# Optimization experiments

Hardware: AMD Instinct MI355X
Metric: run time of the kernel (lower is better)

The kernel has to match this reference:

```python
import jax, jax.numpy as jnp
import numpy as np

DIM = 768
NUM_HEADS = 12
HEAD_DIM = DIM // NUM_HEADS
SCALE = HEAD_DIM ** -0.5


def setup_inputs() -> dict:
    key = jax.random.key(0)
    k1, k2, k3, k4, k5 = jax.random.split(key, 5)
    B, N = 8, 2048
    x = jax.random.normal(k1, (B, N, DIM), dtype=jnp.float32)
    mask = jax.random.randint(k2, (B, N), 0, 2, dtype=jnp.int32)
    # ensure at least one valid key per batch row to avoid all -inf softmax rows
    mask = mask.at[:, 0].set(1)
    w_qkv = jax.random.normal(k3, (DIM, 3 * DIM), dtype=jnp.float32) * (DIM ** -0.5)
    w_proj = jax.random.normal(k4, (DIM, DIM), dtype=jnp.float32) * (DIM ** -0.5)
    b_proj = jax.random.normal(k5, (DIM,), dtype=jnp.float32) * 0.02
    return {"x": x, "mask": mask, "w_qkv": w_qkv, "w_proj": w_proj, "b_proj": b_proj}


def reference(x, mask, w_qkv, w_proj, b_proj):
    B, N, C = x.shape
    qkv = (x @ w_qkv).reshape(B, N, 3, NUM_HEADS, HEAD_DIM)
    qkv = jnp.transpose(qkv, (2, 0, 3, 1, 4))  # [3, B, H, N, D]
    q, k, v = qkv[0], qkv[1], qkv[2]
    q = q * SCALE
    # fp32 upcast for scores (inputs already fp32; explicit for fidelity)
    attn = jnp.einsum('bhqd,bhkd->bhqk', q.astype(jnp.float32), k.astype(jnp.float32))
    key_mask = mask.astype(bool)[:, None, None, :]  # [B,1,1,N]
    attn = jnp.where(key_mask, attn, -jnp.inf)
    attn = jax.nn.softmax(attn, axis=-1).astype(x.dtype)
    out = jnp.einsum('bhqk,bhkd->bhqd', attn, v)  # [B,H,N,D]
    out = jnp.transpose(out, (0, 2, 1, 3)).reshape(B, N, C)
    return out @ w_proj + b_proj
```

## Files before the change

### kernel.cpp

```cpp
#include <hip/hip_runtime.h>
#include <hip/hip_bf16.h>
#include <stdint.h>

#define NHEAD 12
#define SEQ   2048
#define NB    8
#define MTOK  (NB*SEQ)
#define DIMC  768
#define QKVN  (3*DIMC)

typedef __attribute__((ext_vector_type(8))) short bf16x8;
typedef __attribute__((ext_vector_type(4))) float f32x4;
typedef __attribute__((ext_vector_type(16))) float f32x16;
typedef __attribute__((ext_vector_type(4))) unsigned short u16x4;
typedef __attribute__((ext_vector_type(4))) unsigned int u32x4;

typedef const __attribute__((address_space(1))) char glb_char;
typedef __attribute__((address_space(3))) char lds_char;

__device__ __forceinline__ unsigned short f2bf(float f) {
  union { float f; unsigned u; } v; v.f = f;
  return (unsigned short)((v.u + 0x7FFFu + ((v.u >> 16) & 1u)) >> 16);
}

__device__ __forceinline__ void gload_lds16(const void* g, void* l) {
  __builtin_amdgcn_global_load_lds((glb_char*)g, (lds_char*)l, 16, 0, 0);
}

__device__ __forceinline__ unsigned cvtpk_bf16(float lo, float hi) {
  unsigned d;
  asm("v_cvt_pk_bf16_f32 %0, %1, %2" : "=v"(d) : "v"(lo), "v"(hi));
  return d;
}

#define QSCALE 0.18033688011112042f
#define MASKBIAS -30000.0f

__global__ void __launch_bounds__(256, 8)
cvt_bf16_kernel(const float* __restrict__ in,
                unsigned short* __restrict__ out, int n4) {
  int idx = blockIdx.x * blockDim.x + threadIdx.x;
  int stride = gridDim.x * blockDim.x;
  for (int i = idx; i < n4; i += stride) {
    float4 v = ((const float4*)in)[i];
    u16x4 o;
    o.x = f2bf(v.x); o.y = f2bf(v.y); o.z = f2bf(v.z); o.w = f2bf(v.w);
    ((u16x4*)out)[i] = o;
  }
}

__global__ void __launch_bounds__(256, 4)
maskscan_kernel(const int* __restrict__ mask, int* __restrict__ posmap,
                int* __restrict__ srcidx, float* __restrict__ mbias_c,
                int* __restrict__ nvalid) {
  __shared__ int sums[256];
  __shared__ int btot;
  const int b = blockIdx.x, t = threadIdx.x;
  const int* m = mask + b * SEQ;
  int loc[8];
  int s = 0;
  #pragma unroll
  for (int i = 0; i < 8; i++) { loc[i] = (m[t * 8 + i] != 0) ? 1 : 0; s += loc[i]; }
  sums[t] = s;
  __syncthreads();
  for (int off = 1; off < 256; off <<= 1) {
    int v = (t >= off) ? sums[t - off] : 0;
    __syncthreads();
    sums[t] += v;
    __syncthreads();
  }
  int excl = sums[t] - s;
  if (t == 255) btot = sums[255];
  __syncthreads();
  const int nv = btot;
  #pragma unroll
  for (int i = 0; i < 8; i++) {
    posmap[b * SEQ + t * 8 + i] = loc[i] ? excl : -1;
    if (loc[i]) srcidx[b * SEQ + excl] = t * 8 + i;
    excl += loc[i];
  }
  for (int j = t; j < SEQ; j += 256) {
    mbias_c[b * SEQ + j] = (j < nv) ? 0.0f : MASKBIAS;
    if (j >= nv) srcidx[b * SEQ + j] = 0;
  }
  if (t == 0) nvalid[b] = nv;
}

__global__ void __launch_bounds__(256, 8)
transpose_cvt2_kernel(const float* __restrict__ in0, unsigned short* __restrict__ out0,
                      const float* __restrict__ in1, unsigned short* __restrict__ out1) {
  __shared__ float tile[32][33];
  const int z = blockIdx.z;
  const float* in = z ? in1 : in0;
  unsigned short* out = z ? out1 : out0;
  const int C = z ? DIMC : QKVN;
  const int R = DIMC;
  int c0 = blockIdx.x * 32, r0 = blockIdx.y * 32;
  if (c0 >= C) return;
  int tx = threadIdx.x & 31, ty = threadIdx.x >> 5;
  #pragma unroll
  for (int i = 0; i < 32; i += 8)
    tile[ty + i][tx] = in[(size_t)(r0 + ty + i) * C + c0 + tx];
  __syncthreads();
  #pragma unroll
  for (int i = 0; i < 32; i += 8)
    out[(size_t)(c0 + ty + i) * R + r0 + tx] = f2bf(tile[tx][ty + i]);
}

__global__ void __launch_bounds__(256, 3)
qkv_gemm_kernel(const unsigned short* __restrict__ xb,
                const unsigned short* __restrict__ wT,
                unsigned short* __restrict__ qo,
                unsigned short* __restrict__ ko,
                unsigned short* __restrict__ vto,
                const int* __restrict__ srcidx,
                const int* __restrict__ nvalid) {
  __shared__ short lA[3][128 * 32];
  __shared__ short lB[3][128 * 32];
  const int t = threadIdx.x;
  const int lane = t & 63, w = t >> 6;
  const int wr = (w >> 1) * 64, wc = (w & 1) * 64;
  const int l15 = lane & 15, lg = lane >> 4;
  const int sr = t >> 2;
  const int sc = t & 3;
  const int z = blockIdx.z;
  const int NT = DIMC / 32;

  if (z < NB) {
    const int b = z;
    const int m0 = blockIdx.x * 128;
    if (m0 >= ((nvalid[b] + 127) & ~127)) return;
    const int n0 = blockIdx.y * 128;

    const int srow0 = srcidx[b * SEQ + m0 + sr];
    const int srow1 = srcidx[b * SEQ + m0 + 64 + sr];
    const unsigned short* xbb = xb + (size_t)b * SEQ * DIMC;
    const unsigned short* wTkv = wT + (size_t)DIMC * DIMC;

    auto STAGE = [&](int k0, int bsel) {
      int cb = (sc ^ ((sr >> 1) & 3)) * 8;
      gload_lds16(xbb + (size_t)srow0 * DIMC + k0 + cb,
                  (char*)lA + bsel * 8192 + w * 1024);
      gload_lds16(xbb + (size_t)srow1 * DIMC + k0 + cb,
                  (char*)lA + bsel * 8192 + 4096 + w * 1024);
      #pragma unroll
      for (int i = 0; i < 2; i++) {
        int row = i * 64 + sr;
        int cb2 = (sc ^ ((row >> 1) & 3)) * 8;
        gload_lds16(wTkv + (size_t)(n0 + row) * DIMC + k0 + cb2,
                    (char*)lB + bsel * 8192 + i * 4096 + w * 1024);
      }
    };

    f32x4 acc[4][4] = {};
    STAGE(0, 0);
    STAGE(32, 1);
    int cur = 0;
    for (int kt = 0; kt < NT; ++kt) {
      if (kt < NT - 1) asm volatile("s_waitcnt vmcnt(4)" ::: "memory");
      else             asm volatile("s_waitcnt vmcnt(0)" ::: "memory");
      __builtin_amdgcn_s_barrier();
      if (kt + 2 < NT) {
        int nb = cur + 2; if (nb >= 3) nb -= 3;
        STAGE((kt + 2) * 32, nb);
      }
      const short* A = &lA[cur][0];
      const short* B = &lB[cur][0];

      bf16x8 af[4], bfr[4];
      #pragma unroll
      for (int mi = 0; mi < 4; mi++) {
        int m = wr + mi * 16 + l15;
        af[mi] = *(const bf16x8*)&A[m * 32 + ((lg ^ ((m >> 1) & 3)) << 3)];
      }
      #pragma unroll
      for (int nj = 0; nj < 4; nj++) {
        int n = wc + nj * 16 + l15;
        bfr[nj] = *(const bf16x8*)&B[n * 32 + ((lg ^ ((n >> 1) & 3)) << 3)];
      }
      __builtin_amdgcn_s_setprio(1);
      #pragma unroll
      for (int mi = 0; mi < 4; mi++)
        #pragma unroll
        for (int nj = 0; nj < 4; nj++)
          acc[mi][nj] = __builtin_amdgcn_mfma_f32_16x16x32_bf16(af[mi], bfr[nj], acc[mi][nj], 0, 0, 0);
      __builtin_amdgcn_s_setprio(0);

      cur = (cur == 2) ? 0 : cur + 1;
    }

    #pragma unroll
    for (int mi = 0; mi < 4; mi++) {
      int pos0 = m0 + wr + mi * 16 + 4 * lg;
      #pragma unroll
      for (int nj = 0; nj < 4; nj++) {
        int col = n0 + wc + nj * 16 + l15;
        int ch = (col >= DIMC) ? col - DIMC : col;
        int hh = ch >> 6, dd = ch & 63;
        size_t hb = (size_t)(b * NHEAD + hh);
        if (col < DIMC) {
          size_t base = (hb * SEQ + pos0) * 64 + dd;
          #pragma unroll
          for (int r = 0; r < 4; r++)
            ko[base + (size_t)r * 64] = f2bf(acc[mi][nj][r]);
        } else {
          size_t base = (hb * 64 + dd) * SEQ + pos0;
          u16x4 pk;
          pk.x = f2bf(acc[mi][nj][0]); pk.y = f2bf(acc[mi][nj][1]);
          pk.z = f2bf(acc[mi][nj][2]); pk.w = f2bf(acc[mi][nj][3]);
          *(u16x4*)(vto + base) = pk;
        }
      }
    }
  } else {
    const int id = (z - NB) * 192 + blockIdx.y * 16 + blockIdx.x;
    const int m0 = (id / 6) * 128;
    const int n0 = (id % 6) * 128;

    auto STAGE = [&](int k0, int bsel) {
      #pragma unroll
      for (int i = 0; i < 2; i++) {
        int row = i * 64 + sr;
        int cb = (sc ^ ((row >> 1) & 3)) * 8;
        gload_lds16(xb + (size_t)(m0 + row) * DIMC + k0 + cb,
                    (char*)lA + bsel * 8192 + i * 4096 + w * 1024);
        gload_lds16(wT + (size_t)(n0 + row) * DIMC + k0 + cb,
                    (char*)lB + bsel * 8192 + i * 4096 + w * 1024);
      }
    };

    f32x4 acc[4][4] = {};
    STAGE(0, 0);
    STAGE(32, 1);
    int cur = 0;
    for (int kt = 0; kt < NT; ++kt) {
      if (kt < NT - 1) asm volatile("s_waitcnt vmcnt(4)" ::: "memory");
      else             asm volatile("s_waitcnt vmcnt(0)" ::: "memory");
      __builtin_amdgcn_s_barrier();
      if (kt + 2 < NT) {
        int nb = cur + 2; if (nb >= 3) nb -= 3;
        STAGE((kt + 2) * 32, nb);
      }
      const short* A = &lA[cur][0];
      const short* B = &lB[cur][0];

      bf16x8 af[4], bfr[4];
      #pragma unroll
      for (int mi = 0; mi < 4; mi++) {
        int m = wr + mi * 16 + l15;
        af[mi] = *(const bf16x8*)&A[m * 32 + ((lg ^ ((m >> 1) & 3)) << 3)];
      }
      #pragma unroll
      for (int nj = 0; nj < 4; nj++) {
        int n = wc + nj * 16 + l15;
        bfr[nj] = *(const bf16x8*)&B[n * 32 + ((lg ^ ((n >> 1) & 3)) << 3)];
      }
      __builtin_amdgcn_s_setprio(1);
      #pragma unroll
      for (int mi = 0; mi < 4; mi++)
        #pragma unroll
        for (int nj = 0; nj < 4; nj++)
          acc[mi][nj] = __builtin_amdgcn_mfma_f32_16x16x32_bf16(af[mi], bfr[nj], acc[mi][nj], 0, 0, 0);
      __builtin_amdgcn_s_setprio(0);

      cur = (cur == 2) ? 0 : cur + 1;
    }

    #pragma unroll
    for (int mi = 0; mi < 4; mi++) {
      int tok0 = m0 + wr + mi * 16 + 4 * lg;
      int bb = tok0 >> 11;
      int nn0 = tok0 & 2047;
      #pragma unroll
      for (int nj = 0; nj < 4; nj++) {
        int col = n0 + wc + nj * 16 + l15;
        int hh = col >> 6, dd = col & 63;
        size_t base = (((size_t)(bb * NHEAD + hh)) * SEQ + nn0) * 64 + dd;
        #pragma unroll
        for (int r = 0; r < 4; r++)
          qo[base + (size_t)r * 64] = f2bf(acc[mi][nj][r] * QSCALE);
      }
    }
  }
}

__global__ void __launch_bounds__(256, 4)
attn_kernel(const unsigned short* __restrict__ qbuf,
            const unsigned short* __restrict__ kbuf,
            const unsigned short* __restrict__ vtbuf,
            const float* __restrict__ mbias_c,
            const int* __restrict__ nvalid,
            unsigned short* __restrict__ ao) {
  __shared__ short lKV[2][8192];
  __shared__ float lmask[2][64];
  const int t = threadIdx.x, lane = t & 63, w = t >> 6;
  const int l31 = lane & 31, hi = lane >> 5;
  const int bid = blockIdx.x;
  const int qt = bid / 96;
  const int bh = bid - qt * 96;
  const int b = bh / NHEAD, h = bh - b * NHEAD;
  const int q0 = qt * 128 + w * 32;
  const unsigned short* qb = qbuf + (size_t)bh * SEQ * 64;
  const unsigned short* kb = kbuf + (size_t)bh * SEQ * 64;
  const unsigned short* vb = vtbuf + (size_t)bh * 64 * SEQ;
  const float* mb = mbias_c + b * SEQ;
  const int ntiles = (nvalid[b] + 63) >> 6;

  auto STAGE = [&](int tile, int bsel) {
    int kv0 = tile * 64;
    #pragma unroll
    for (int i = 0; i < 2; i++) {
      int c = i * 4 + w;
      gload_lds16(kb + (size_t)(kv0 + lane) * 64 + c * 8,
                  (char*)lKV + bsel * 16384 + c * 1024);
      gload_lds16(vb + (size_t)lane * SEQ + kv0 + c * 8,
                  (char*)lKV + bsel * 16384 + 8192 + c * 1024);
    }
    if (w == 0)
      __builtin_amdgcn_global_load_lds((glb_char*)(mb + tile * 64 + lane),
                                       (lds_char*)&lmask[bsel][0], 4, 0, 0);
  };

  bf16x8 qf[4];
  #pragma unroll
  for (int dblk = 0; dblk < 4; dblk++)
    qf[dblk] = *(const bf16x8*)(qb + (size_t)(q0 + l31) * 64 + dblk * 16 + hi * 8);

  f32x16 O[2] = {};
  float ls[4] = {0.f, 0.f, 0.f, 0.f};

  STAGE(0, 0);
  __syncthreads();

  for (int it = 0; it < ntiles; ++it) {
    const int bsel = it & 1;
    const short* Kb = &lKV[bsel][0];
    const short* Vb = &lKV[bsel][4096];
    if (it + 1 < ntiles) STAGE(it + 1, bsel ^ 1);

    #pragma unroll
    for (int kb2 = 0; kb2 < 2; kb2++) {
      f32x4 mb4[4];
      #pragma unroll
      for (int g = 0; g < 4; g++)
        mb4[g] = *(const f32x4*)&lmask[bsel][kb2 * 32 + g * 8 + hi * 4];
      f32x16 S;
      #pragma unroll
      for (int r = 0; r < 16; r++) S[r] = mb4[r >> 2][r & 3];

      __builtin_amdgcn_s_setprio(1);
      #pragma unroll
      for (int dblk = 0; dblk < 4; dblk++) {
        bf16x8 kf = *(const bf16x8*)&Kb[(dblk * 2 + hi) * 512 + (kb2 * 32 + l31) * 8];
        S = __builtin_amdgcn_mfma_f32_32x32x16_bf16(kf, qf[dblk], S, 0, 0, 0);
      }
      __builtin_amdgcn_s_setprio(0);

      float p[16];
      #pragma unroll
      for (int r = 0; r < 16; r++) p[r] = __builtin_amdgcn_exp2f(S[r]);
      #pragma unroll
      for (int r = 0; r < 16; r++) ls[r & 3] += p[r];

      #pragma unroll
      for (int half = 0; half < 2; half++) {
        unsigned a0 = cvtpk_bf16(p[half * 8 + 0], p[half * 8 + 1]);
        unsigned a1 = cvtpk_bf16(p[half * 8 + 2], p[half * 8 + 3]);
        unsigned a2 = cvtpk_bf16(p[half * 8 + 4], p[half * 8 + 5]);
        unsigned a3 = cvtpk_bf16(p[half * 8 + 6], p[half * 8 + 7]);
        asm("v_permlane32_swap_b32 %0, %1" : "+v"(a0), "+v"(a2));
        asm("v_permlane32_swap_b32 %0, %1" : "+v"(a1), "+v"(a3));
        union { u32x4 u; bf16x8 f; } cv;
        cv.u = (u32x4){a0, a1, a2, a3};
        __builtin_amdgcn_s_setprio(1);
        #pragma unroll
        for (int dt = 0; dt < 2; dt++) {
          bf16x8 vf = *(const bf16x8*)&Vb[(kb2 * 4 + half * 2 + hi) * 512 + (dt * 32 + l31) * 8];
          O[dt] = __builtin_amdgcn_mfma_f32_32x32x16_bf16(cv.f, vf, O[dt], 0, 0, 0);
        }
        __builtin_amdgcn_s_setprio(0);
      }
    }

    if (it + 1 < ntiles) {
      asm volatile("s_waitcnt vmcnt(0)" ::: "memory");
      __builtin_amdgcn_s_barrier();
    }
  }

  __syncthreads();
  float* lrs = (float*)&lKV[0][0];
  float tot = (ls[0] + ls[1]) + (ls[2] + ls[3]);
  tot += __shfl_xor(tot, 32);
  lrs[w * 32 + l31] = tot;

  float inv[16];
  #pragma unroll
  for (int r = 0; r < 16; r++)
    inv[r] = 1.0f / lrs[w * 32 + (r & 3) + 8 * (r >> 2) + 4 * hi];

  #pragma unroll
  for (int dt = 0; dt < 2; dt++) {
    #pragma unroll
    for (int r = 0; r < 16; r++) {
      int qrow = q0 + (r & 3) + 8 * (r >> 2) + 4 * hi;
      size_t base = ((size_t)(b * SEQ + qrow)) * DIMC + h * 64 + dt * 32 + l31;
      ao[base] = __bfloat16_as_ushort(__float2bfloat16(O[dt][r] * inv[r]));
    }
  }
}

__global__ void __launch_bounds__(256, 3)
proj_gemm_kernel(const unsigned short* __restrict__ ab,
                 const unsigned short* __restrict__ wT,
                 const float* __restrict__ bias,
                 float* __restrict__ out) {
  __shared__ short lA[3][128 * 32];
  __shared__ short lB[3][128 * 32];
  const int t = threadIdx.x;
  const int lane = t & 63, w = t >> 6;
  const int m0 = blockIdx.x * 128;
  const int n0 = blockIdx.y * 128;
  const int wr = (w >> 1) * 64, wc = (w & 1) * 64;
  const int l15 = lane & 15, lg = lane >> 4;
  const int sr = t >> 2;
  const int sc = t & 3;

  auto STAGE = [&](int k0, int bsel) {
    #pragma unroll
    for (int i = 0; i < 2; i++) {
      int row = i * 64 + sr;
      int cb = (sc ^ ((row >> 1) & 3)) * 8;
      gload_lds16(ab + (size_t)(m0 + row) * DIMC + k0 + cb,
                  (char*)lA + bsel * 8192 + i * 4096 + w * 1024);
      gload_lds16(wT + (size_t)(n0 + row) * DIMC + k0 + cb,
                  (char*)lB + bsel * 8192 + i * 4096 + w * 1024);
    }
  };

  f32x4 acc[4][4] = {};
  const int NT = DIMC / 32;

  STAGE(0, 0);
  STAGE(32, 1);

  int cur = 0;
  for (int kt = 0; kt < NT; ++kt) {
    if (kt < NT - 1) asm volatile("s_waitcnt vmcnt(4)" ::: "memory");
    else             asm volatile("s_waitcnt vmcnt(0)" ::: "memory");
    __builtin_amdgcn_s_barrier();
    if (kt + 2 < NT) {
      int nb = cur + 2; if (nb >= 3) nb -= 3;
      STAGE((kt + 2) * 32, nb);
    }
    const short* A = &lA[cur][0];
    const short* B = &lB[cur][0];

    bf16x8 af[4], bfr[4];
    #pragma unroll
    for (int mi = 0; mi < 4; mi++) {
      int m = wr + mi * 16 + l15;
      af[mi] = *(const bf16x8*)&A[m * 32 + ((lg ^ ((m >> 1) & 3)) << 3)];
    }
    #pragma unroll
    for (int nj = 0; nj < 4; nj++) {
      int n = wc + nj * 16 + l15;
      bfr[nj] = *(const bf16x8*)&B[n * 32 + ((lg ^ ((n >> 1) & 3)) << 3)];
    }
    __builtin_amdgcn_s_setprio(1);
    #pragma unroll
    for (int mi = 0; mi < 4; mi++)
      #pragma unroll
      for (int nj = 0; nj < 4; nj++)
        acc[mi][nj] = __builtin_amdgcn_mfma_f32_16x16x32_bf16(af[mi], bfr[nj], acc[mi][nj], 0, 0, 0);
    __builtin_amdgcn_s_setprio(0);

    cur = (cur == 2) ? 0 : cur + 1;
  }

  #pragma unroll
  for (int mi = 0; mi < 4; mi++) {
    int row0 = m0 + wr + mi * 16 + 4 * lg;
    #pragma unroll
    for (int nj = 0; nj < 4; nj++) {
      int col = n0 + wc + nj * 16 + l15;
      float bv = bias[col];
      #pragma unroll
      for (int r = 0; r < 4; r++)
        out[(size_t)(row0 + r) * DIMC + col] = acc[mi][nj][r] + bv;
    }
  }
}

extern "C" void kernel_launch(void* const* d_in, const int* in_sizes, int n_in,
                              void* d_out, int out_size, void* d_ws, size_t ws_size,
                              hipStream_t stream) {
  const float* x      = (const float*)d_in[0];
  const int*   mask   = (const int*)d_in[1];
  const float* w_qkv  = (const float*)d_in[2];
  const float* w_proj = (const float*)d_in[3];
  const float* b_proj = (const float*)d_in[4];
  float* out = (float*)d_out;

  unsigned short* ws = (unsigned short*)d_ws;
  unsigned short* xb     = ws;
  unsigned short* wqkvT  = xb    + (size_t)MTOK * DIMC;
  unsigned short* wprojT = wqkvT + (size_t)QKVN * DIMC;
  unsigned short* qbuf   = wprojT + (size_t)DIMC * DIMC;
  unsigned short* kbuf   = qbuf  + (size_t)MTOK * DIMC;
  unsigned short* vtbuf  = kbuf  + (size_t)MTOK * DIMC;
  float*          mbias_c = (float*)(vtbuf + (size_t)MTOK * DIMC);
  int*            posmap  = (int*)(mbias_c + MTOK);
  int*            nvalid  = posmap + MTOK;
  int*            srcidx  = nvalid + 8;
  unsigned short* aob    = xb;

  cvt_bf16_kernel<<<2048, 256, 0, stream>>>(x, xb, MTOK * DIMC / 4);
  maskscan_kernel<<<NB, 256, 0, stream>>>(mask, posmap, srcidx, mbias_c, nvalid);
  transpose_cvt2_kernel<<<dim3(QKVN / 32, DIMC / 32, 2), 256, 0, stream>>>(w_qkv, wqkvT, w_proj, wprojT);
  qkv_gemm_kernel<<<dim3(16, 12, 12), 256, 0, stream>>>(xb, wqkvT, qbuf, kbuf, vtbuf, srcidx, nvalid);
  attn_kernel<<<1536, 256, 0, stream>>>(qbuf, kbuf, vtbuf, mbias_c, nvalid, aob);
  proj_gemm_kernel<<<dim3(128, 6), 256, 0, stream>>>(aob, wprojT, b_proj, out);
}
```

Measured before the change: 196.5 us.

## Load K, V and mask directly from global memory in attention kernel

Removes the double-buffered LDS staging of K/V tiles and the mask in the attention kernel. Each wave now reads its K, V and mask fragments straight from global memory (relying on L1/L2), which drops the per-tile barriers and waitcnts. The launch bound occupancy hint is lowered from 4 to 3. The trade is that the four waves of a block now each fetch the same K/V data through the cache hierarchy instead of sharing one LDS copy. Loads are no longer prefetched a tile ahead, so their latency may be exposed.

After: 359.4 us. +82.9%, slower.

```diff
diff --git a/kernel.cpp b/kernel.cpp
--- a/kernel.cpp
+++ b/kernel.cpp
@@ -284,15 +284,14 @@
   }
 }
 
-__global__ void __launch_bounds__(256, 4)
+__global__ void __launch_bounds__(256, 3)
 attn_kernel(const unsigned short* __restrict__ qbuf,
             const unsigned short* __restrict__ kbuf,
             const unsigned short* __restrict__ vtbuf,
             const float* __restrict__ mbias_c,
             const int* __restrict__ nvalid,
             unsigned short* __restrict__ ao) {
-  __shared__ short lKV[2][8192];
-  __shared__ float lmask[2][64];
+  __shared__ float lrs[4][32];
   const int t = threadIdx.x, lane = t & 63, w = t >> 6;
   const int l31 = lane & 31, hi = lane >> 5;
   const int bid = blockIdx.x;
@@ -306,21 +305,6 @@
   const float* mb = mbias_c + b * SEQ;
   const int ntiles = (nvalid[b] + 63) >> 6;
 
-  auto STAGE = [&](int tile, int bsel) {
-    int kv0 = tile * 64;
-    #pragma unroll
-    for (int i = 0; i < 2; i++) {
-      int c = i * 4 + w;
-      gload_lds16(kb + (size_t)(kv0 + lane) * 64 + c * 8,
-                  (char*)lKV + bsel * 16384 + c * 1024);
-      gload_lds16(vb + (size_t)lane * SEQ + kv0 + c * 8,
-                  (char*)lKV + bsel * 16384 + 8192 + c * 1024);
-    }
-    if (w == 0)
-      __builtin_amdgcn_global_load_lds((glb_char*)(mb + tile * 64 + lane),
-                                       (lds_char*)&lmask[bsel][0], 4, 0, 0);
-  };
-
   bf16x8 qf[4];
   #pragma unroll
   for (int dblk = 0; dblk < 4; dblk++)
@@ -329,21 +313,15 @@
   f32x16 O[2] = {};
   float ls[4] = {0.f, 0.f, 0.f, 0.f};
 
-  STAGE(0, 0);
-  __syncthreads();
-
   for (int it = 0; it < ntiles; ++it) {
-    const int bsel = it & 1;
-    const short* Kb = &lKV[bsel][0];
-    const short* Vb = &lKV[bsel][4096];
-    if (it + 1 < ntiles) STAGE(it + 1, bsel ^ 1);
+    const int kv0 = it * 64;
 
     #pragma unroll
     for (int kb2 = 0; kb2 < 2; kb2++) {
       f32x4 mb4[4];
       #pragma unroll
       for (int g = 0; g < 4; g++)
-        mb4[g] = *(const f32x4*)&lmask[bsel][kb2 * 32 + g * 8 + hi * 4];
+        mb4[g] = *(const f32x4*)(mb + kv0 + kb2 * 32 + g * 8 + hi * 4);
       f32x16 S;
       #pragma unroll
       for (int r = 0; r < 16; r++) S[r] = mb4[r >> 2][r & 3];
@@ -351,7 +329,7 @@
       __builtin_amdgcn_s_setprio(1);
       #pragma unroll
       for (int dblk = 0; dblk < 4; dblk++) {
-        bf16x8 kf = *(const bf16x8*)&Kb[(dblk * 2 + hi) * 512 + (kb2 * 32 + l31) * 8];
+        bf16x8 kf = *(const bf16x8*)(kb + (size_t)(kv0 + kb2 * 32 + l31) * 64 + (dblk * 2 + hi) * 8);
         S = __builtin_amdgcn_mfma_f32_32x32x16_bf16(kf, qf[dblk], S, 0, 0, 0);
       }
       __builtin_amdgcn_s_setprio(0);
@@ -375,29 +353,22 @@
         __builtin_amdgcn_s_setprio(1);
         #pragma unroll
         for (int dt = 0; dt < 2; dt++) {
-          bf16x8 vf = *(const bf16x8*)&Vb[(kb2 * 4 + half * 2 + hi) * 512 + (dt * 32 + l31) * 8];
+          bf16x8 vf = *(const bf16x8*)(vb + (size_t)(dt * 32 + l31) * SEQ + kv0 + (kb2 * 4 + half * 2 + hi) * 8);
           O[dt] = __builtin_amdgcn_mfma_f32_32x32x16_bf16(cv.f, vf, O[dt], 0, 0, 0);
         }
         __builtin_amdgcn_s_setprio(0);
       }
     }
-
-    if (it + 1 < ntiles) {
-      asm volatile("s_waitcnt vmcnt(0)" ::: "memory");
-      __builtin_amdgcn_s_barrier();
-    }
-  }
-
-  __syncthreads();
-  float* lrs = (float*)&lKV[0][0];
+  }
+
   float tot = (ls[0] + ls[1]) + (ls[2] + ls[3]);
   tot += __shfl_xor(tot, 32);
-  lrs[w * 32 + l31] = tot;
+  lrs[w][l31] = tot;
 
   float inv[16];
   #pragma unroll
   for (int r = 0; r < 16; r++)
-    inv[r] = 1.0f / lrs[w * 32 + (r & 3) + 8 * (r >> 2) + 4 * hi];
+    inv[r] = 1.0f / lrs[w][(r & 3) + 8 * (r >> 2) + 4 * hi];
 
   #pragma unroll
   for (int dt = 0; dt < 2; dt++) {
```
